# Optimization experiments

Hardware: AMD Instinct MI355X
Metric: run time of the kernel (lower is better)

Reference implementation:

```python
import jax, jax.numpy as jnp
import numpy as np

T, D, K, V, NB = 32768, 256, 16, 16, 2
H = K * V  # hidden size; must equal D for the residual x + y

def phi(x):
    return 1.0 + jax.nn.elu(x)

def _layernorm(x, w, b, eps=1e-5):
    m = x.mean(-1, keepdims=True)
    v = ((x - m) ** 2).mean(-1, keepdims=True)
    return (x - m) * jax.lax.rsqrt(v + eps) * w + b

def _combine(a, b):
    # reset-wrapped associative update: right element's start flag zeroes the left carry
    pa, sa, za = a
    pb, sb, zb = b
    keep = jnp.logical_not(pb)
    return (jnp.logical_or(pa, pb), keep * sa + sb, keep * za + zb)

def _block(x, start, s0, z0, Wk, Wq, Wv, bv, Wskip, bskip, Wm1, bm1, Wm2, bm2, Wm3, bm3, lnw, lnb):
    k = phi(x @ Wk.T)                                   # [T,K]
    q = phi(x @ Wq.T)                                   # [T,K]
    v = x @ Wv.T + bv                                   # [T,V]
    kv = jnp.einsum('ti,tj->tij', k, v)                 # [T,K,V]
    s = jnp.concatenate([s0, kv], axis=0)               # [T+1,K,V]
    z = jnp.concatenate([z0, k[:, None, :]], axis=0)    # [T+1,1,K]
    st = jnp.concatenate([jnp.zeros((1, 1, 1), bool), start.reshape(-1, 1, 1)], axis=0)
    _, s, z = jax.lax.associative_scan(_combine, (st, s, z), axis=0)
    s, z = s[1:], z[1:]
    numer = jnp.einsum('tij,ti->tj', s, q)              # [T,V]
    denom = jnp.einsum('tzi,tj->tz', z, q).clip(1e-6)   # [T,1] (faithful to source einsum)
    out = numer / denom                                 # [T,V]
    h = jax.nn.leaky_relu(out @ Wm1.T + bm1)
    h = jax.nn.leaky_relu(h @ Wm2.T + bm2)
    h = h @ Wm3.T + bm3
    return _layernorm(h + (x @ Wskip.T + bskip), lnw, lnb)

def _forward(x, start, s0, z0, Wk, Wq, Wv, bv, Wskip, bskip, Wm1, bm1, Wm2, bm2, Wm3, bm3, lnw, lnb):
    y = x
    for i in range(NB):  # small fixed layer loop
        y = _block(x, start, s0[i], z0[i], Wk[i], Wq[i], Wv[i], bv[i], Wskip[i], bskip[i],
                   Wm1[i], bm1[i], Wm2[i], bm2[i], Wm3[i], bm3[i], lnw[i], lnb[i])
        x = x + y
    return y

def setup_inputs() -> dict:
    key = jax.random.key(0)
    ks = jax.random.split(key, 12)
    g = lambda k, shp, fan: jax.random.normal(k, shp, jnp.float32) * (fan ** -0.5)
    return dict(
        x=jax.random.normal(ks[0], (T, D), jnp.float32),
        start=jax.random.randint(ks[1], (T,), 0, 2).astype(bool),
        s0=jnp.zeros((NB, 1, K, V), jnp.float32),
        z0=jnp.zeros((NB, 1, 1, K), jnp.float32),
        Wk=g(ks[2], (NB, K, D), D), Wq=g(ks[3], (NB, K, D), D),
        Wv=g(ks[4], (NB, V, D), D), bv=jnp.zeros((NB, V), jnp.float32),
        Wskip=g(ks[5], (NB, H, D), D), bskip=jnp.zeros((NB, H), jnp.float32),
        Wm1=g(ks[6], (NB, H, V), V), bm1=jnp.zeros((NB, H), jnp.float32),
        Wm2=g(ks[7], (NB, H, H), H), bm2=jnp.zeros((NB, H), jnp.float32),
        Wm3=g(ks[8], (NB, H, H), H), bm3=jnp.zeros((NB, H), jnp.float32),
        ln_w=jnp.ones((NB, H), jnp.float32), ln_b=jnp.zeros((NB, H), jnp.float32),
    )

def reference(x, start, s0, z0, Wk, Wq, Wv, bv, Wskip, bskip, Wm1, bm1, Wm2, bm2, Wm3, bm3, ln_w, ln_b):
    return _forward(x, start, s0, z0, Wk, Wq, Wv, bv, Wskip, bskip, Wm1, bm1, Wm2, bm2, Wm3, bm3, ln_w, ln_b)
```

## Files before the change

### kernel.cpp

```cpp
#include <hip/hip_runtime.h>
#include <hip/hip_bf16.h>
#include <cstdint>

#define TT   32768
#define DD   256
#define KV   16
#define NBLK 2
#define HH   256
#define CH   64
#define NCH  (TT / CH)

typedef __attribute__((ext_vector_type(8))) short bf16x8;
typedef __attribute__((ext_vector_type(4))) float f32x4;

__device__ __forceinline__ float phi_f(float x)  { return x > 0.f ? x + 1.f : expf(x); }
__device__ __forceinline__ float lrelu_f(float x){ return x > 0.f ? x : 0.01f * x; }
__device__ __forceinline__ unsigned short f2bf(float f) {
  unsigned u = __float_as_uint(f);
  u += 0x7fffu + ((u >> 16) & 1u);
  return (unsigned short)(u >> 16);
}
__device__ __forceinline__ float bf2f(unsigned short h) {
  return __uint_as_float(((unsigned)h) << 16);
}

__global__ void k_detect(const void* __restrict__ startp, int* __restrict__ flags) {
  int stride = gridDim.x * blockDim.x;
  for (int t = blockIdx.x * blockDim.x + threadIdx.x; t < TT / 4; t += stride) {
    unsigned u = ((const unsigned*)startp)[t];
    if (u > 1u) atomicOr(&flags[0], 1);
    float f = ((const float*)startp)[t];
    if (!(f == 0.f || f == 1.f)) atomicOr(&flags[1], 1);
  }
}

__global__ void k_canon(const void* __restrict__ startp, const int* __restrict__ flags,
                        float* __restrict__ start_f) {
  int v32 = flags[0], vf = flags[1];
  int stride = gridDim.x * blockDim.x;
  for (int t = blockIdx.x * blockDim.x + threadIdx.x; t < TT; t += stride) {
    bool s;
    if (v32 == 0)     s = ((const unsigned*)startp)[t] != 0u;
    else if (vf == 0) s = ((const float*)startp)[t] != 0.f;
    else              s = ((const unsigned char*)startp)[t] != 0;
    start_f[t] = s ? 1.f : 0.f;
  }
}

__global__ __launch_bounds__(256) void k_cvtbig(
    const float* __restrict__ s0, const float* __restrict__ s1, const float* __restrict__ s2,
    unsigned short* __restrict__ d0, unsigned short* __restrict__ d1,
    unsigned short* __restrict__ d2, int n) {
  int i = (blockIdx.x * 256 + threadIdx.x) * 8;
  const float* s; unsigned short* d;
  if (i < n)            { s = s0; d = d0; }
  else if (i < 2 * n)   { s = s1; d = d1; i -= n; }
  else if (i < 3 * n)   { s = s2; d = d2; i -= 2 * n; }
  else return;
  float4 a = *(const float4*)(s + i);
  float4 b = *(const float4*)(s + i + 4);
  float vals[8] = {a.x, a.y, a.z, a.w, b.x, b.y, b.z, b.w};
  bf16x8 t;
#pragma unroll
  for (int j = 0; j < 8; j++) t[j] = (short)f2bf(vals[j]);
  *(bf16x8*)(d + i) = t;
}

__global__ __launch_bounds__(256) void k_cvtproj(
    const float* __restrict__ Wk, const float* __restrict__ Wq, const float* __restrict__ Wv,
    unsigned short* __restrict__ wh, unsigned short* __restrict__ wl) {
  int t8 = blockIdx.x * 256 + threadIdx.x;
  if (t8 >= NBLK * 48 * 256 / 8) return;
  int e = t8 * 8;
  int b = e / (48 * 256);
  int rem = e - b * 48 * 256;
  int o = rem / (16 * 256);
  int nr = rem - o * 16 * 256;
  const float* src = (o == 0 ? Wk : o == 1 ? Wq : Wv) + b * 16 * 256 + nr;
  float4 a = *(const float4*)src;
  float4 c = *(const float4*)(src + 4);
  float vals[8] = {a.x, a.y, a.z, a.w, c.x, c.y, c.z, c.w};
  bf16x8 th, tl;
#pragma unroll
  for (int j = 0; j < 8; j++) {
    unsigned short h = f2bf(vals[j]);
    th[j] = (short)h;
    tl[j] = (short)f2bf(vals[j] - bf2f(h));
  }
  *(bf16x8*)(wh + e) = th;
  *(bf16x8*)(wl + e) = tl;
}

__global__ __launch_bounds__(256) void k_cvtm1(
    const float* __restrict__ Wm1,
    unsigned short* __restrict__ h, unsigned short* __restrict__ l) {
  int row = blockIdx.x * 256 + threadIdx.x;
  if (row >= NBLK * 256) return;
  const float* s = Wm1 + row * 16;
  bf16x8 th0, tl0, th1, tl1, z;
#pragma unroll
  for (int j = 0; j < 8; j++) {
    float v0 = s[j], v1 = s[j + 8];
    unsigned short h0 = f2bf(v0), h1 = f2bf(v1);
    th0[j] = (short)h0; tl0[j] = (short)f2bf(v0 - bf2f(h0));
    th1[j] = (short)h1; tl1[j] = (short)f2bf(v1 - bf2f(h1));
    z[j] = 0;
  }
  unsigned short* dh = h + row * 32;
  unsigned short* dl = l + row * 32;
  *(bf16x8*)(dh) = th0;  *(bf16x8*)(dh + 8) = th1;
  *(bf16x8*)(dh + 16) = z; *(bf16x8*)(dh + 24) = z;
  *(bf16x8*)(dl) = tl0;  *(bf16x8*)(dl + 8) = tl1;
  *(bf16x8*)(dl + 16) = z; *(bf16x8*)(dl + 24) = z;
}

__global__ __launch_bounds__(256) void k_proj2(
    const float* __restrict__ x,
    const unsigned short* __restrict__ wh, const unsigned short* __restrict__ wl,
    const float* __restrict__ bv,
    float* __restrict__ kout, float* __restrict__ qout, float* __restrict__ vout) {
  __shared__ unsigned short xh[64 * 256];
  __shared__ unsigned short xl[64 * 256];
  int tid = threadIdx.x, wg = blockIdx.x;
  size_t rbase = (size_t)wg * 64;
  const float* xs = x + rbase * DD;
#pragma unroll
  for (int i = 0; i < 8; i++) {
    int idx = tid + i * 256;
    int row = idx >> 5, c8 = idx & 31;
    const float* p = xs + row * DD + c8 * 8;
    float4 a = *(const float4*)p;
    float4 b = *(const float4*)(p + 4);
    float vals[8] = {a.x, a.y, a.z, a.w, b.x, b.y, b.z, b.w};
    bf16x8 th, tl;
#pragma unroll
    for (int j = 0; j < 8; j++) {
      unsigned short h = f2bf(vals[j]);
      th[j] = (short)h;
      tl[j] = (short)f2bf(vals[j] - bf2f(h));
    }
    int off = row * 512 + ((c8 * 16) ^ ((row & 7) << 4));
    *(bf16x8*)((char*)xh + off) = th;
    *(bf16x8*)((char*)xl + off) = tl;
  }
  __syncthreads();

  int lane = tid & 63, wv = tid >> 6, lg = lane >> 4, lr = lane & 15;
  int r = wv * 16 + lr;
  f32x4 acc[3];
#pragma unroll
  for (int o = 0; o < 3; o++) acc[o] = (f32x4){0.f, 0.f, 0.f, 0.f};

#pragma unroll
  for (int kk = 0; kk < 8; kk++) {
    int kbyte = kk * 64 + lg * 16;
    int off = r * 512 + (kbyte ^ ((r & 7) << 4));
    bf16x8 ah = *(bf16x8*)((char*)xh + off);
    bf16x8 al = *(bf16x8*)((char*)xl + off);
#pragma unroll
    for (int o = 0; o < 3; o++) {
      bf16x8 bh = *(const bf16x8*)((const char*)wh + (o * 16 + lr) * 512 + kbyte);
      bf16x8 bl = *(const bf16x8*)((const char*)wl + (o * 16 + lr) * 512 + kbyte);
      acc[o] = __builtin_amdgcn_mfma_f32_16x16x32_bf16(ah, bh, acc[o], 0, 0, 0);
      acc[o] = __builtin_amdgcn_mfma_f32_16x16x32_bf16(al, bh, acc[o], 0, 0, 0);
      acc[o] = __builtin_amdgcn_mfma_f32_16x16x32_bf16(ah, bl, acc[o], 0, 0, 0);
    }
  }
  float bvv = bv[lr];
#pragma unroll
  for (int rg = 0; rg < 4; rg++) {
    size_t g = rbase + wv * 16 + lg * 4 + rg;
    kout[g * KV + lr] = phi_f(acc[0][rg]);
    qout[g * KV + lr] = phi_f(acc[1][rg]);
    vout[g * KV + lr] = acc[2][rg] + bvv;
  }
}

__global__ __launch_bounds__(256) void k_tails(
    const float* __restrict__ k, const float* __restrict__ v,
    const float* __restrict__ start_f,
    float* __restrict__ tails_s, float* __restrict__ tails_zs,
    float* __restrict__ tails_flag) {
  __shared__ float kc[CH * KV], vc[CH * KV], stc[CH], red[CH];
  __shared__ int lsS;
  int c = blockIdx.x, tid = threadIdx.x;
  const float* kp = k + (size_t)c * CH * KV;
  const float* vp = v + (size_t)c * CH * KV;
  for (int u = tid; u < CH * KV; u += 256) { kc[u] = kp[u]; vc[u] = vp[u]; }
  if (tid < CH) stc[tid] = start_f[c * CH + tid];
  __syncthreads();
  if (tid == 0) {
    int ls = -1;
    for (int t = 0; t < CH; t++) if (stc[t] != 0.f) ls = t;
    lsS = ls;
  }
  __syncthreads();
  int ls = lsS;
  int t0 = ls < 0 ? 0 : ls;
  int i = tid >> 4, j = tid & 15;
  float s = 0.f;
  for (int t = t0; t < CH; t++) s += kc[t * KV + i] * vc[t * KV + j];
  tails_s[(size_t)c * 256 + tid] = s;
  if (tid < CH) {
    float r = 0.f;
    if (tid >= t0) {
      for (int i2 = 0; i2 < KV; i2++) r += kc[tid * KV + i2];
    }
    red[tid] = r;
  }
  __syncthreads();
  if (tid == 0) {
    float z = 0.f;
    for (int t = 0; t < CH; t++) z += red[t];
    tails_zs[c] = z;
    tails_flag[c] = (ls >= 0) ? 1.f : 0.f;
  }
}

#define SP 65
__global__ __launch_bounds__(256) void k_att(
    const float* __restrict__ q, const float* __restrict__ k,
    const float* __restrict__ v, const float* __restrict__ start_f,
    const float* __restrict__ tails_s, const float* __restrict__ tails_zs,
    const float* __restrict__ tails_flag,
    const float* __restrict__ s0, const float* __restrict__ z0,
    float* __restrict__ att) {
  __shared__ float qc[CH * KV], kc[CH * KV], vc[CH * KV], stc[CH];
  __shared__ float S[CH * SP];
  __shared__ float carry[256];
  __shared__ float ksum[CH], zsl[CH], qsum[CH];
  __shared__ int ns[CH];
  __shared__ float czs_s;
  int c = blockIdx.x, tid = threadIdx.x;
  size_t base = (size_t)c * CH * KV;
  for (int u = tid; u < CH * KV; u += 256) {
    qc[u] = q[base + u]; kc[u] = k[base + u]; vc[u] = v[base + u];
  }
  if (tid < CH) stc[tid] = start_f[c * CH + tid];
  __syncthreads();
  if (tid < CH) {
    int cnt = 0;
    for (int u = 0; u <= tid; u++) cnt += (stc[u] != 0.f);
    ns[tid] = cnt;
    float ks = 0.f, qs = 0.f;
    for (int i = 0; i < KV; i++) { ks += kc[tid * KV + i]; qs += qc[tid * KV + i]; }
    ksum[tid] = ks; qsum[tid] = qs;
  }
  __syncthreads();
  if (tid < CH) {
    float acc = 0.f;
    for (int u = tid; u >= 0; u--) { acc += ksum[u]; if (stc[u] != 0.f) break; }
    zsl[tid] = acc;
  }
  {
    float accs = 0.f, aczs = 0.f;
    int cc = c - 1;
    for (;;) {
      if (cc < 0) {
        accs += s0[tid];
        if (tid == 0) { float z = 0.f; for (int i = 0; i < KV; i++) z += z0[i]; aczs += z; }
        break;
      }
      float fl = tails_flag[cc];
      accs += tails_s[(size_t)cc * 256 + tid];
      if (tid == 0) aczs += tails_zs[cc];
      if (fl != 0.f) break;
      cc--;
    }
    carry[tid] = accs;
    if (tid == 0) czs_s = aczs;
  }
  __syncthreads();
  {
    int t = tid >> 2, g = tid & 3;
    for (int u = 0; u < 16; u++) {
      int tp = g * 16 + u;
      float val = 0.f;
      if (tp <= t && ns[tp] == ns[t]) {
        float dot = 0.f;
        for (int i = 0; i < KV; i++) dot += qc[t * KV + i] * kc[tp * KV + i];
        val = dot;
      }
      S[t * SP + tp] = val;
    }
  }
  __syncthreads();
  float czs = czs_s;
  int j = tid & 15, tr = tid >> 4;
  for (int p = 0; p < 4; p++) {
    int t = p * 16 + tr;
    float numer = 0.f;
    for (int tp = 0; tp < CH; tp++) numer += S[t * SP + tp] * vc[tp * KV + j];
    float zs = zsl[t];
    if (ns[t] == 0) {
      float cn = 0.f;
      for (int i = 0; i < KV; i++) cn += qc[t * KV + i] * carry[i * KV + j];
      numer += cn;
      zs += czs;
    }
    float denom = fmaxf(zs * qsum[t], 1e-6f);
    att[base + t * KV + j] = numer / denom;
  }
}

#define A1S 40
template<int WY, int WX>
__global__ __launch_bounds__(512, 4) void k_mlp4(
    const float* __restrict__ att, const float* __restrict__ xsrc,
    const unsigned short* __restrict__ wm1h, const unsigned short* __restrict__ wm1l,
    const float* __restrict__ bm1,
    const unsigned short* __restrict__ Wm2b, const float* __restrict__ bm2,
    const unsigned short* __restrict__ Wm3b, const float* __restrict__ bm3,
    const unsigned short* __restrict__ Wskb, const float* __restrict__ bsk,
    const float* __restrict__ lnw, const float* __restrict__ lnb,
    float* __restrict__ yout, float* __restrict__ xnext) {
  __shared__ unsigned short hb[64 * 256];
  __shared__ __align__(16) char uni[64 * A1S * 4];
  unsigned short* aoh = (unsigned short*)uni;
  unsigned short* aol = aoh + 64 * A1S;
  float* redS = (float*)uni;
  float* redQ = redS + 512;
  float* mrow = redQ + 512;
  float* irow = mrow + 64;

  int tid = threadIdx.x, wg = blockIdx.x;
  size_t rbase = (size_t)wg * 64;

  for (int idx = tid; idx < 64 * 32; idx += 512) {
    int row = idx >> 5, col = idx & 31;
    float v = (col < 16) ? att[(rbase + row) * KV + col] : 0.f;
    unsigned short h = f2bf(v);
    aoh[row * A1S + col] = h;
    aol[row * A1S + col] = f2bf(v - bf2f(h));
  }
  __syncthreads();

  int lane = tid & 63, wv = tid >> 6, lg = lane >> 4, lr = lane & 15;
  int nc0 = wv * 32;

  f32x4 acc[4][2];
#pragma unroll
  for (int a = 0; a < 4; a++)
#pragma unroll
    for (int b = 0; b < 2; b++) acc[a][b] = (f32x4){0.f, 0.f, 0.f, 0.f};

  {
    bf16x8 b1h[2], b1l[2];
#pragma unroll
    for (int nt = 0; nt < 2; nt++) {
      int n = nc0 + nt * 16 + lr;
      b1h[nt] = *(const bf16x8*)(wm1h + n * 32 + lg * 8);
      b1l[nt] = *(const bf16x8*)(wm1l + n * 32 + lg * 8);
    }
#pragma unroll
    for (int mt = 0; mt < 4; mt++) {
      int r = mt * 16 + lr;
      bf16x8 ah = *(bf16x8*)(aoh + r * A1S + lg * 8);
      bf16x8 al = *(bf16x8*)(aol + r * A1S + lg * 8);
#pragma unroll
      for (int nt = 0; nt < 2; nt++) {
        acc[mt][nt] = __builtin_amdgcn_mfma_f32_16x16x32_bf16(ah, b1h[nt], acc[mt][nt], 0, 0, 0);
        acc[mt][nt] = __builtin_amdgcn_mfma_f32_16x16x32_bf16(al, b1h[nt], acc[mt][nt], 0, 0, 0);
        acc[mt][nt] = __builtin_amdgcn_mfma_f32_16x16x32_bf16(ah, b1l[nt], acc[mt][nt], 0, 0, 0);
      }
    }
  }
  __syncthreads();
  {
    float bm1v[2];
#pragma unroll
    for (int nt = 0; nt < 2; nt++) bm1v[nt] = bm1[nc0 + nt * 16 + lr];
#pragma unroll
    for (int mt = 0; mt < 4; mt++)
#pragma unroll
      for (int nt = 0; nt < 2; nt++)
#pragma unroll
        for (int rg = 0; rg < 4; rg++) {
          int r = mt * 16 + lg * 4 + rg;
          int cc = nc0 + nt * 16 + lr;
          *(unsigned short*)((char*)hb + r * 512 + ((cc * 2) ^ ((r & 7) << 4))) =
              f2bf(lrelu_f(acc[mt][nt][rg] + bm1v[nt]));
        }
  }
  __syncthreads();

#pragma unroll
  for (int a = 0; a < 4; a++)
#pragma unroll
    for (int b = 0; b < 2; b++) acc[a][b] = (f32x4){0.f, 0.f, 0.f, 0.f};
  for (int kk = 0; kk < 8; kk++) {
    int kbyte = kk * 64 + lg * 16;
    bf16x8 bfr[2];
#pragma unroll
    for (int nt = 0; nt < 2; nt++) {
      int n = nc0 + nt * 16 + lr;
      bfr[nt] = *(const bf16x8*)((const char*)Wm2b + n * 512 + kbyte);
    }
#pragma unroll
    for (int mt = 0; mt < 4; mt++) {
      int r = mt * 16 + lr;
      bf16x8 af = *(bf16x8*)((char*)hb + r * 512 + (kbyte ^ ((r & 7) << 4)));
#pragma unroll
      for (int nt = 0; nt < 2; nt++)
        acc[mt][nt] = __builtin_amdgcn_mfma_f32_16x16x32_bf16(af, bfr[nt], acc[mt][nt], 0, 0, 0);
    }
  }
  __syncthreads();
  {
    float bm2v[2];
#pragma unroll
    for (int nt = 0; nt < 2; nt++) bm2v[nt] = bm2[nc0 + nt * 16 + lr];
#pragma unroll
    for (int mt = 0; mt < 4; mt++)
#pragma unroll
      for (int nt = 0; nt < 2; nt++)
#pragma unroll
        for (int rg = 0; rg < 4; rg++) {
          int r = mt * 16 + lg * 4 + rg;
          int cc = nc0 + nt * 16 + lr;
          *(unsigned short*)((char*)hb + r * 512 + ((cc * 2) ^ ((r & 7) << 4))) =
              f2bf(lrelu_f(acc[mt][nt][rg] + bm2v[nt]));
        }
  }
  __syncthreads();

  f32x4 acc2[4][2];
#pragma unroll
  for (int a = 0; a < 4; a++)
#pragma unroll
    for (int b = 0; b < 2; b++) acc2[a][b] = (f32x4){0.f, 0.f, 0.f, 0.f};
  const float* xrow = xsrc + rbase * DD;
  for (int kk = 0; kk < 8; kk++) {
    int kbyte = kk * 64 + lg * 16;
    int kf = kk * 32 + lg * 8;
    bf16x8 b3[2], bs[2];
#pragma unroll
    for (int nt = 0; nt < 2; nt++) {
      int n = nc0 + nt * 16 + lr;
      b3[nt] = *(const bf16x8*)((const char*)Wm3b + n * 512 + kbyte);
      bs[nt] = *(const bf16x8*)((const char*)Wskb + n * 512 + kbyte);
    }
#pragma unroll
    for (int mt = 0; mt < 4; mt++) {
      int r = mt * 16 + lr;
      bf16x8 a2 = *(bf16x8*)((char*)hb + r * 512 + (kbyte ^ ((r & 7) << 4)));
#pragma unroll
      for (int nt = 0; nt < 2; nt++)
        acc2[mt][nt] = __builtin_amdgcn_mfma_f32_16x16x32_bf16(a2, b3[nt], acc2[mt][nt], 0, 0, 0);
      const float* xp = xrow + r * DD + kf;
      float4 x0 = *(const float4*)xp;
      float4 x1 = *(const float4*)(xp + 4);
      bf16x8 xv;
      xv[0] = (short)f2bf(x0.x); xv[1] = (short)f2bf(x0.y);
      xv[2] = (short)f2bf(x0.z); xv[3] = (short)f2bf(x0.w);
      xv[4] = (short)f2bf(x1.x); xv[5] = (short)f2bf(x1.y);
      xv[6] = (short)f2bf(x1.z); xv[7] = (short)f2bf(x1.w);
#pragma unroll
      for (int nt = 0; nt < 2; nt++)
        acc2[mt][nt] = __builtin_amdgcn_mfma_f32_16x16x32_bf16(xv, bs[nt], acc2[mt][nt], 0, 0, 0);
    }
  }
#pragma unroll
  for (int nt = 0; nt < 2; nt++) {
    int cc = nc0 + nt * 16 + lr;
    float bb = bm3[cc] + bsk[cc];
#pragma unroll
    for (int mt = 0; mt < 4; mt++)
#pragma unroll
      for (int rg = 0; rg < 4; rg++) acc2[mt][nt][rg] += bb;
  }

#pragma unroll
  for (int mt = 0; mt < 4; mt++)
#pragma unroll
    for (int rg = 0; rg < 4; rg++) {
      float s = 0.f, q = 0.f;
#pragma unroll
      for (int nt = 0; nt < 2; nt++) {
        float v = acc2[mt][nt][rg];
        s += v; q += v * v;
      }
#pragma unroll
      for (int m = 1; m < 16; m <<= 1) {
        s += __shfl_xor(s, m);
        q += __shfl_xor(q, m);
      }
      if (lr == 0) {
        int r = mt * 16 + lg * 4 + rg;
        redS[wv * 64 + r] = s;
        redQ[wv * 64 + r] = q;
      }
    }
  __syncthreads();
  if (tid < 64) {
    float s = 0.f, q = 0.f;
#pragma unroll
    for (int w = 0; w < 8; w++) { s += redS[w * 64 + tid]; q += redQ[w * 64 + tid]; }
    float m = s * (1.f / 256.f);
    float var = q * (1.f / 256.f) - m * m;
    mrow[tid] = m;
    irow[tid] = rsqrtf(var + 1e-5f);
  }
  __syncthreads();

  {
    float lnwv[2], lnbv[2];
#pragma unroll
    for (int nt = 0; nt < 2; nt++) {
      int cc = nc0 + nt * 16 + lr;
      lnwv[nt] = lnw[cc]; lnbv[nt] = lnb[cc];
    }
#pragma unroll
    for (int mt = 0; mt < 4; mt++)
#pragma unroll
      for (int rg = 0; rg < 4; rg++) {
        int r = mt * 16 + lg * 4 + rg;
        float m = mrow[r], is = irow[r];
        size_t gr = (rbase + r) * DD;
#pragma unroll
        for (int nt = 0; nt < 2; nt++) {
          int cc = nc0 + nt * 16 + lr;
          float y = (acc2[mt][nt][rg] - m) * is * lnwv[nt] + lnbv[nt];
          if (WY) yout[gr + cc] = y;
          if (WX) xnext[gr + cc] = xsrc[gr + cc] + y;
        }
      }
  }
}

extern "C" void kernel_launch(void* const* d_in, const int* in_sizes, int n_in,
                              void* d_out, int out_size, void* d_ws, size_t ws_size,
                              hipStream_t stream) {
  const float* x_in = (const float*)d_in[0];
  const void*  startp = d_in[1];
  const float* s0  = (const float*)d_in[2];
  const float* z0  = (const float*)d_in[3];
  const float* Wk  = (const float*)d_in[4];
  const float* Wq  = (const float*)d_in[5];
  const float* Wv  = (const float*)d_in[6];
  const float* bv  = (const float*)d_in[7];
  const float* Wsk = (const float*)d_in[8];
  const float* bsk = (const float*)d_in[9];
  const float* Wm1 = (const float*)d_in[10];
  const float* bm1 = (const float*)d_in[11];
  const float* Wm2 = (const float*)d_in[12];
  const float* bm2 = (const float*)d_in[13];
  const float* Wm3 = (const float*)d_in[14];
  const float* bm3 = (const float*)d_in[15];
  const float* lnw = (const float*)d_in[16];
  const float* lnb = (const float*)d_in[17];
  float* yout = (float*)d_out;

  float* ws = (float*)d_ws;
  int*   flags   = (int*)d_ws;
  float* start_f = ws + 16;
  float* kbuf    = start_f + TT;
  float* qbuf    = kbuf + (size_t)TT * KV;
  float* vbuf    = qbuf + (size_t)TT * KV;
  float* abuf    = vbuf + (size_t)TT * KV;
  float* ts      = abuf + (size_t)TT * KV;
  float* tz      = ts + (size_t)NCH * 256;
  float* tf      = tz + NCH;
  float* xcur    = tf + NCH;
  unsigned short* wm2b = (unsigned short*)(xcur + (size_t)TT * DD);
  unsigned short* wm3b = wm2b + (size_t)NBLK * HH * HH;
  unsigned short* wskb = wm3b + (size_t)NBLK * HH * HH;
  unsigned short* wpjh = wskb + (size_t)NBLK * HH * DD;
  unsigned short* wpjl = wpjh + (size_t)NBLK * 48 * DD;
  unsigned short* wm1h = wpjl + (size_t)NBLK * 48 * DD;
  unsigned short* wm1l = wm1h + (size_t)NBLK * HH * 32;

  hipMemsetAsync(d_ws, 0, 64, stream);
  k_detect<<<64, 256, 0, stream>>>(startp, flags);
  k_canon<<<256, 256, 0, stream>>>(startp, flags, start_f);

  k_cvtbig<<<192, 256, 0, stream>>>(Wm2, Wm3, Wsk, wm2b, wm3b, wskb, NBLK * HH * HH);
  k_cvtproj<<<12, 256, 0, stream>>>(Wk, Wq, Wv, wpjh, wpjl);
  k_cvtm1<<<2, 256, 0, stream>>>(Wm1, wm1h, wm1l);

  const float* xs = x_in;
  for (int b = 0; b < NBLK; b++) {
    k_proj2<<<TT / 64, 256, 0, stream>>>(xs,
        wpjh + (size_t)b * 48 * DD, wpjl + (size_t)b * 48 * DD,
        bv + (size_t)b * KV, kbuf, qbuf, vbuf);
    k_tails<<<NCH, 256, 0, stream>>>(kbuf, vbuf, start_f, ts, tz, tf);
    k_att<<<NCH, 256, 0, stream>>>(qbuf, kbuf, vbuf, start_f, ts, tz, tf,
        s0 + (size_t)b * 256, z0 + (size_t)b * KV, abuf);
    if (b == 0) {
      k_mlp4<0, 1><<<TT / 64, 512, 0, stream>>>(abuf, xs,
          wm1h + (size_t)b * HH * 32, wm1l + (size_t)b * HH * 32, bm1 + (size_t)b * HH,
          wm2b + (size_t)b * HH * HH, bm2 + (size_t)b * HH,
          wm3b + (size_t)b * HH * HH, bm3 + (size_t)b * HH,
          wskb + (size_t)b * HH * DD, bsk + (size_t)b * HH,
          lnw + (size_t)b * HH, lnb + (size_t)b * HH, yout, xcur);
    } else {
      k_mlp4<1, 0><<<TT / 64, 512, 0, stream>>>(abuf, xs,
          wm1h + (size_t)b * HH * 32, wm1l + (size_t)b * HH * 32, bm1 + (size_t)b * HH,
          wm2b + (size_t)b * HH * HH, bm2 + (size_t)b * HH,
          wm3b + (size_t)b * HH * HH, bm3 + (size_t)b * HH,
          wskb + (size_t)b * HH * DD, bsk + (size_t)b * HH,
          lnw + (size_t)b * HH, lnb + (size_t)b * HH, yout, xcur);
    }
    xs = xcur;
  }
}
```

Before: 319.7 us.

## Fuse chunk-tail computation into projection kernel and widen MLP per-wave tiles

The per-chunk tail reduction (last reset position, k⊗v tail sum, k-sum) now runs inside the projection kernel. It reuses the freshly computed k/v staged in shared memory, which removes a separate launch and a global reload of k and v. The last-start search uses a wave ballot, and the z-sum uses a shuffle reduction. Separately, the MLP kernel drops from 512 to 256 threads per block, with each wave covering 64 output columns instead of 32 and the k-loops fully unrolled. This gives more B-fragment reuse per A load, at the cost of doubled accumulator registers and possibly lower occupancy.

```diff
diff --git a/kernel.cpp b/kernel.cpp
--- a/kernel.cpp
+++ b/kernel.cpp
@@ -114,13 +114,20 @@
   *(bf16x8*)(dl + 16) = z; *(bf16x8*)(dl + 24) = z;
 }
 
-__global__ __launch_bounds__(256) void k_proj2(
+__global__ __launch_bounds__(256) void k_projt(
     const float* __restrict__ x,
     const unsigned short* __restrict__ wh, const unsigned short* __restrict__ wl,
-    const float* __restrict__ bv,
-    float* __restrict__ kout, float* __restrict__ qout, float* __restrict__ vout) {
+    const float* __restrict__ bv, const float* __restrict__ start_f,
+    float* __restrict__ kout, float* __restrict__ qout, float* __restrict__ vout,
+    float* __restrict__ tails_s, float* __restrict__ tails_zs,
+    float* __restrict__ tails_flag) {
   __shared__ unsigned short xh[64 * 256];
   __shared__ unsigned short xl[64 * 256];
+  __shared__ float stc[CH];
+  __shared__ int lsS;
+  float* kc = (float*)xh;
+  float* vc = kc + 64 * 16;
+
   int tid = threadIdx.x, wg = blockIdx.x;
   size_t rbase = (size_t)wg * 64;
   const float* xs = x + rbase * DD;
@@ -143,6 +150,7 @@
     *(bf16x8*)((char*)xh + off) = th;
     *(bf16x8*)((char*)xl + off) = tl;
   }
+  if (tid < CH) stc[tid] = start_f[wg * CH + tid];
   __syncthreads();
 
   int lane = tid & 63, wv = tid >> 6, lg = lane >> 4, lr = lane & 15;
@@ -166,54 +174,46 @@
       acc[o] = __builtin_amdgcn_mfma_f32_16x16x32_bf16(ah, bl, acc[o], 0, 0, 0);
     }
   }
+  __syncthreads();
+
   float bvv = bv[lr];
 #pragma unroll
   for (int rg = 0; rg < 4; rg++) {
-    size_t g = rbase + wv * 16 + lg * 4 + rg;
-    kout[g * KV + lr] = phi_f(acc[0][rg]);
+    int rl = wv * 16 + lg * 4 + rg;
+    size_t g = rbase + rl;
+    float kvl = phi_f(acc[0][rg]);
+    float vvl = acc[2][rg] + bvv;
+    kout[g * KV + lr] = kvl;
     qout[g * KV + lr] = phi_f(acc[1][rg]);
-    vout[g * KV + lr] = acc[2][rg] + bvv;
-  }
-}
-
-__global__ __launch_bounds__(256) void k_tails(
-    const float* __restrict__ k, const float* __restrict__ v,
-    const float* __restrict__ start_f,
-    float* __restrict__ tails_s, float* __restrict__ tails_zs,
-    float* __restrict__ tails_flag) {
-  __shared__ float kc[CH * KV], vc[CH * KV], stc[CH], red[CH];
-  __shared__ int lsS;
-  int c = blockIdx.x, tid = threadIdx.x;
-  const float* kp = k + (size_t)c * CH * KV;
-  const float* vp = v + (size_t)c * CH * KV;
-  for (int u = tid; u < CH * KV; u += 256) { kc[u] = kp[u]; vc[u] = vp[u]; }
-  if (tid < CH) stc[tid] = start_f[c * CH + tid];
-  __syncthreads();
-  if (tid == 0) {
-    int ls = -1;
-    for (int t = 0; t < CH; t++) if (stc[t] != 0.f) ls = t;
-    lsS = ls;
+    vout[g * KV + lr] = vvl;
+    kc[rl * KV + lr] = kvl;
+    vc[rl * KV + lr] = vvl;
+  }
+  if (tid < 64) {
+    unsigned long long mask = __ballot(stc[tid] != 0.f);
+    if (tid == 0) lsS = mask ? (63 - __builtin_clzll(mask)) : -1;
   }
   __syncthreads();
   int ls = lsS;
   int t0 = ls < 0 ? 0 : ls;
-  int i = tid >> 4, j = tid & 15;
-  float s = 0.f;
-  for (int t = t0; t < CH; t++) s += kc[t * KV + i] * vc[t * KV + j];
-  tails_s[(size_t)c * 256 + tid] = s;
-  if (tid < CH) {
-    float r = 0.f;
+  {
+    int i = tid >> 4, j = tid & 15;
+    float s = 0.f;
+    for (int t = t0; t < CH; t++) s += kc[t * KV + i] * vc[t * KV + j];
+    tails_s[(size_t)wg * 256 + tid] = s;
+  }
+  if (tid < 64) {
+    float ks = 0.f;
     if (tid >= t0) {
-      for (int i2 = 0; i2 < KV; i2++) r += kc[tid * KV + i2];
-    }
-    red[tid] = r;
-  }
-  __syncthreads();
-  if (tid == 0) {
-    float z = 0.f;
-    for (int t = 0; t < CH; t++) z += red[t];
-    tails_zs[c] = z;
-    tails_flag[c] = (ls >= 0) ? 1.f : 0.f;
+#pragma unroll
+      for (int i = 0; i < KV; i++) ks += kc[tid * KV + i];
+    }
+#pragma unroll
+    for (int m = 1; m < 64; m <<= 1) ks += __shfl_xor(ks, m);
+    if (tid == 0) {
+      tails_zs[wg] = ks;
+      tails_flag[wg] = (ls >= 0) ? 1.f : 0.f;
+    }
   }
 }
 
@@ -305,7 +305,7 @@
 
 #define A1S 40
 template<int WY, int WX>
-__global__ __launch_bounds__(512, 4) void k_mlp4(
+__global__ __launch_bounds__(256, 2) void k_mlp5(
     const float* __restrict__ att, const float* __restrict__ xsrc,
     const unsigned short* __restrict__ wm1h, const unsigned short* __restrict__ wm1l,
     const float* __restrict__ bm1,
@@ -319,14 +319,14 @@
   unsigned short* aoh = (unsigned short*)uni;
   unsigned short* aol = aoh + 64 * A1S;
   float* redS = (float*)uni;
-  float* redQ = redS + 512;
-  float* mrow = redQ + 512;
+  float* redQ = redS + 256;
+  float* mrow = redQ + 256;
   float* irow = mrow + 64;
 
   int tid = threadIdx.x, wg = blockIdx.x;
   size_t rbase = (size_t)wg * 64;
 
-  for (int idx = tid; idx < 64 * 32; idx += 512) {
+  for (int idx = tid; idx < 64 * 32; idx += 256) {
     int row = idx >> 5, col = idx & 31;
     float v = (col < 16) ? att[(rbase + row) * KV + col] : 0.f;
     unsigned short h = f2bf(v);
@@ -336,18 +336,18 @@
   __syncthreads();
 
   int lane = tid & 63, wv = tid >> 6, lg = lane >> 4, lr = lane & 15;
-  int nc0 = wv * 32;
-
-  f32x4 acc[4][2];
+  int nc0 = wv * 64;
+
+  f32x4 acc[4][4];
 #pragma unroll
   for (int a = 0; a < 4; a++)
 #pragma unroll
-    for (int b = 0; b < 2; b++) acc[a][b] = (f32x4){0.f, 0.f, 0.f, 0.f};
+    for (int b = 0; b < 4; b++) acc[a][b] = (f32x4){0.f, 0.f, 0.f, 0.f};
 
   {
-    bf16x8 b1h[2], b1l[2];
-#pragma unroll
-    for (int nt = 0; nt < 2; nt++) {
+    bf16x8 b1h[4], b1l[4];
+#pragma unroll
+    for (int nt = 0; nt < 4; nt++) {
       int n = nc0 + nt * 16 + lr;
       b1h[nt] = *(const bf16x8*)(wm1h + n * 32 + lg * 8);
       b1l[nt] = *(const bf16x8*)(wm1l + n * 32 + lg * 8);
@@ -358,7 +358,7 @@
       bf16x8 ah = *(bf16x8*)(aoh + r * A1S + lg * 8);
       bf16x8 al = *(bf16x8*)(aol + r * A1S + lg * 8);
 #pragma unroll
-      for (int nt = 0; nt < 2; nt++) {
+      for (int nt = 0; nt < 4; nt++) {
         acc[mt][nt] = __builtin_amdgcn_mfma_f32_16x16x32_bf16(ah, b1h[nt], acc[mt][nt], 0, 0, 0);
         acc[mt][nt] = __builtin_amdgcn_mfma_f32_16x16x32_bf16(al, b1h[nt], acc[mt][nt], 0, 0, 0);
         acc[mt][nt] = __builtin_amdgcn_mfma_f32_16x16x32_bf16(ah, b1l[nt], acc[mt][nt], 0, 0, 0);
@@ -367,13 +367,13 @@
   }
   __syncthreads();
   {
-    float bm1v[2];
-#pragma unroll
-    for (int nt = 0; nt < 2; nt++) bm1v[nt] = bm1[nc0 + nt * 16 + lr];
+    float bm1v[4];
+#pragma unroll
+    for (int nt = 0; nt < 4; nt++) bm1v[nt] = bm1[nc0 + nt * 16 + lr];
 #pragma unroll
     for (int mt = 0; mt < 4; mt++)
 #pragma unroll
-      for (int nt = 0; nt < 2; nt++)
+      for (int nt = 0; nt < 4; nt++)
 #pragma unroll
         for (int rg = 0; rg < 4; rg++) {
           int r = mt * 16 + lg * 4 + rg;
@@ -387,12 +387,13 @@
 #pragma unroll
   for (int a = 0; a < 4; a++)
 #pragma unroll
-    for (int b = 0; b < 2; b++) acc[a][b] = (f32x4){0.f, 0.f, 0.f, 0.f};
+    for (int b = 0; b < 4; b++) acc[a][b] = (f32x4){0.f, 0.f, 0.f, 0.f};
+#pragma unroll
   for (int kk = 0; kk < 8; kk++) {
     int kbyte = kk * 64 + lg * 16;
-    bf16x8 bfr[2];
-#pragma unroll
-    for (int nt = 0; nt < 2; nt++) {
+    bf16x8 bfr[4];
+#pragma unroll
+    for (int nt = 0; nt < 4; nt++) {
       int n = nc0 + nt * 16 + lr;
       bfr[nt] = *(const bf16x8*)((const char*)Wm2b + n * 512 + kbyte);
     }
@@ -401,19 +402,19 @@
       int r = mt * 16 + lr;
       bf16x8 af = *(bf16x8*)((char*)hb + r * 512 + (kbyte ^ ((r & 7) << 4)));
 #pragma unroll
-      for (int nt = 0; nt < 2; nt++)
+      for (int nt = 0; nt < 4; nt++)
         acc[mt][nt] = __builtin_amdgcn_mfma_f32_16x16x32_bf16(af, bfr[nt], acc[mt][nt], 0, 0, 0);
     }
   }
   __syncthreads();
   {
-    float bm2v[2];
-#pragma unroll
-    for (int nt = 0; nt < 2; nt++) bm2v[nt] = bm2[nc0 + nt * 16 + lr];
+    float bm2v[4];
+#pragma unroll
+    for (int nt = 0; nt < 4; nt++) bm2v[nt] = bm2[nc0 + nt * 16 + lr];
 #pragma unroll
     for (int mt = 0; mt < 4; mt++)
 #pragma unroll
-      for (int nt = 0; nt < 2; nt++)
+      for (int nt = 0; nt < 4; nt++)
 #pragma unroll
         for (int rg = 0; rg < 4; rg++) {
           int r = mt * 16 + lg * 4 + rg;
@@ -424,18 +425,19 @@
   }
   __syncthreads();
 
-  f32x4 acc2[4][2];
+  f32x4 acc2[4][4];
 #pragma unroll
   for (int a = 0; a < 4; a++)
 #pragma unroll
-    for (int b = 0; b < 2; b++) acc2[a][b] = (f32x4){0.f, 0.f, 0.f, 0.f};
+    for (int b = 0; b < 4; b++) acc2[a][b] = (f32x4){0.f, 0.f, 0.f, 0.f};
   const float* xrow = xsrc + rbase * DD;
+#pragma unroll
   for (int kk = 0; kk < 8; kk++) {
     int kbyte = kk * 64 + lg * 16;
     int kf = kk * 32 + lg * 8;
-    bf16x8 b3[2], bs[2];
-#pragma unroll
-    for (int nt = 0; nt < 2; nt++) {
+    bf16x8 b3[4], bs[4];
+#pragma unroll
+    for (int nt = 0; nt < 4; nt++) {
       int n = nc0 + nt * 16 + lr;
       b3[nt] = *(const bf16x8*)((const char*)Wm3b + n * 512 + kbyte);
       bs[nt] = *(const bf16x8*)((const char*)Wskb + n * 512 + kbyte);
@@ -445,7 +447,7 @@
       int r = mt * 16 + lr;
       bf16x8 a2 = *(bf16x8*)((char*)hb + r * 512 + (kbyte ^ ((r & 7) << 4)));
 #pragma unroll
-      for (int nt = 0; nt < 2; nt++)
+      for (int nt = 0; nt < 4; nt++)
         acc2[mt][nt] = __builtin_amdgcn_mfma_f32_16x16x32_bf16(a2, b3[nt], acc2[mt][nt], 0, 0, 0);
       const float* xp = xrow + r * DD + kf;
       float4 x0 = *(const float4*)xp;
@@ -456,12 +458,12 @@
       xv[4] = (short)f2bf(x1.x); xv[5] = (short)f2bf(x1.y);
       xv[6] = (short)f2bf(x1.z); xv[7] = (short)f2bf(x1.w);
 #pragma unroll
-      for (int nt = 0; nt < 2; nt++)
+      for (int nt = 0; nt < 4; nt++)
         acc2[mt][nt] = __builtin_amdgcn_mfma_f32_16x16x32_bf16(xv, bs[nt], acc2[mt][nt], 0, 0, 0);
     }
   }
 #pragma unroll
-  for (int nt = 0; nt < 2; nt++) {
+  for (int nt = 0; nt < 4; nt++) {
     int cc = nc0 + nt * 16 + lr;
     float bb = bm3[cc] + bsk[cc];
 #pragma unroll
@@ -476,7 +478,7 @@
     for (int rg = 0; rg < 4; rg++) {
       float s = 0.f, q = 0.f;
 #pragma unroll
-      for (int nt = 0; nt < 2; nt++) {
+      for (int nt = 0; nt < 4; nt++) {
         float v = acc2[mt][nt][rg];
         s += v; q += v * v;
       }
@@ -495,7 +497,7 @@
   if (tid < 64) {
     float s = 0.f, q = 0.f;
 #pragma unroll
-    for (int w = 0; w < 8; w++) { s += redS[w * 64 + tid]; q += redQ[w * 64 + tid]; }
+    for (int w = 0; w < 4; w++) { s += redS[w * 64 + tid]; q += redQ[w * 64 + tid]; }
     float m = s * (1.f / 256.f);
     float var = q * (1.f / 256.f) - m * m;
     mrow[tid] = m;
@@ -504,9 +506,9 @@
   __syncthreads();
 
   {
-    float lnwv[2], lnbv[2];
-#pragma unroll
-    for (int nt = 0; nt < 2; nt++) {
+    float lnwv[4], lnbv[4];
+#pragma unroll
+    for (int nt = 0; nt < 4; nt++) {
       int cc = nc0 + nt * 16 + lr;
       lnwv[nt] = lnw[cc]; lnbv[nt] = lnb[cc];
     }
@@ -518,7 +520,7 @@
         float m = mrow[r], is = irow[r];
         size_t gr = (rbase + r) * DD;
 #pragma unroll
-        for (int nt = 0; nt < 2; nt++) {
+        for (int nt = 0; nt < 4; nt++) {
           int cc = nc0 + nt * 16 + lr;
           float y = (acc2[mt][nt][rg] - m) * is * lnwv[nt] + lnbv[nt];
           if (WY) yout[gr + cc] = y;
@@ -580,21 +582,20 @@
 
   const float* xs = x_in;
   for (int b = 0; b < NBLK; b++) {
-    k_proj2<<<TT / 64, 256, 0, stream>>>(xs,
+    k_projt<<<TT / 64, 256, 0, stream>>>(xs,
         wpjh + (size_t)b * 48 * DD, wpjl + (size_t)b * 48 * DD,
-        bv + (size_t)b * KV, kbuf, qbuf, vbuf);
-    k_tails<<<NCH, 256, 0, stream>>>(kbuf, vbuf, start_f, ts, tz, tf);
+        bv + (size_t)b * KV, start_f, kbuf, qbuf, vbuf, ts, tz, tf);
     k_att<<<NCH, 256, 0, stream>>>(qbuf, kbuf, vbuf, start_f, ts, tz, tf,
         s0 + (size_t)b * 256, z0 + (size_t)b * KV, abuf);
     if (b == 0) {
-      k_mlp4<0, 1><<<TT / 64, 512, 0, stream>>>(abuf, xs,
+      k_mlp5<0, 1><<<TT / 64, 256, 0, stream>>>(abuf, xs,
           wm1h + (size_t)b * HH * 32, wm1l + (size_t)b * HH * 32, bm1 + (size_t)b * HH,
           wm2b + (size_t)b * HH * HH, bm2 + (size_t)b * HH,
           wm3b + (size_t)b * HH * HH, bm3 + (size_t)b * HH,
           wskb + (size_t)b * HH * DD, bsk + (size_t)b * HH,
           lnw + (size_t)b * HH, lnb + (size_t)b * HH, yout, xcur);
     } else {
-      k_mlp4<1, 0><<<TT / 64, 512, 0, stream>>>(abuf, xs,
+      k_mlp5<1, 0><<<TT / 64, 256, 0, stream>>>(abuf, xs,
           wm1h + (size_t)b * HH * 32, wm1l + (size_t)b * HH * 32, bm1 + (size_t)b * HH,
           wm2b + (size_t)b * HH * HH, bm2 + (size_t)b * HH,
           wm3b + (size_t)b * HH * HH, bm3 + (size_t)b * HH,
```

After: 289.6 us. -9.4%, faster.
